# Kernel tuning notes

Hardware: AMD Instinct MI355X
Metric: run time of the kernel (lower is better)

## Reference

```python
import jax, jax.numpy as jnp
import numpy as np

B, S, D, H = 2, 2048, 1024, 16
DH = D // H  # 64


def setup_inputs() -> dict:
    key = jax.random.key(0)
    k1, k2, k3 = jax.random.split(key, 3)
    return {
        "x": jax.random.normal(k1, (B, S, D), dtype=jnp.float32),
        "w_qkv": jax.random.normal(k2, (D, 3 * D), dtype=jnp.float32) * 0.02,
        "b_qkv": jnp.zeros((3 * D,), dtype=jnp.float32),
        "w_out": jax.random.normal(k3, (D, D), dtype=jnp.float32) * 0.02,
        "b_out": jnp.zeros((D,), dtype=jnp.float32),
    }


def reference(x, w_qkv, b_qkv, w_out, b_out):
    # fused qkv projection: [B,S,3D]
    qkv = x @ w_qkv + b_qkv
    q, k, v = qkv[..., :D], qkv[..., D:2 * D], qkv[..., 2 * D:]
    # split heads -> [B,H,S,DH]
    split = lambda t: t.reshape(B, S, H, DH).transpose(0, 2, 1, 3)
    q, k, v = split(q), split(k), split(v)
    scale = 1.0 / jnp.sqrt(jnp.asarray(DH, dtype=x.dtype))
    scores = jnp.einsum("bhqd,bhkd->bhqk", q, k) * scale  # [B,H,S,S]
    attn = jax.nn.softmax(scores, axis=-1)
    out = jnp.einsum("bhqk,bhkd->bhqd", attn, v)  # [B,H,S,DH]
    out = out.transpose(0, 2, 1, 3).reshape(B, S, D)
    return out @ w_out + b_out
```

## Files before the change

kernel.cpp:

```cpp
#include <hip/hip_runtime.h>
#include <cstdint>

#define B_ 2
#define S_ 2048
#define D_ 1024
#define H_ 16
#define DH_ 64

typedef short bf16x8 __attribute__((ext_vector_type(8)));
typedef float f32x4 __attribute__((ext_vector_type(4)));

__device__ inline unsigned short f2bf(float f) {
  unsigned int u = __float_as_uint(f);
  u += 0x7fffu + ((u >> 16) & 1u);
  return (unsigned short)(u >> 16);
}

__device__ inline float bf2f(unsigned short h) {
  return __uint_as_float(((unsigned int)h) << 16);
}

__device__ inline float fexp2(float x) { return __builtin_amdgcn_exp2f(x); }

__device__ inline int swz(int row, int bytecol) {
  return row * 128 + (bytecol ^ ((row & 7) << 4));
}

#define GLL(gp, lp)                                                            \
  __builtin_amdgcn_global_load_lds(                                            \
      (const __attribute__((address_space(1))) unsigned int*)(gp),             \
      (__attribute__((address_space(3))) unsigned int*)(lp), 16, 0, 0)

__global__ __launch_bounds__(256) void k_prep(const float* __restrict__ x,
                                              unsigned short* __restrict__ xb,
                                              const float* __restrict__ w_qkv,
                                              unsigned short* __restrict__ wqT,
                                              const float* __restrict__ w_out,
                                              unsigned short* __restrict__ woT) {
  __shared__ float tile[32][33];
  const int bid = blockIdx.x;
  const int t = threadIdx.x;
  if (bid < 4096) {
    int i = bid * 256 + t;
    float4 v = reinterpret_cast<const float4*>(x)[i];
    ushort4 o;
    o.x = f2bf(v.x); o.y = f2bf(v.y); o.z = f2bf(v.z); o.w = f2bf(v.w);
    reinterpret_cast<ushort4*>(xb)[i] = o;
    return;
  }
  const float* in;
  unsigned short* out;
  int R, C, bx, by;
  if (bid < 7168) {
    int id = bid - 4096;
    bx = id % 96; by = id / 96;
    in = w_qkv; out = wqT; R = 1024; C = 3072;
  } else {
    int id = bid - 7168;
    bx = id & 31; by = id >> 5;
    in = w_out; out = woT; R = 1024; C = 1024;
  }
  int ct = bx * 32, rt = by * 32;
  int tx = t & 31, ty = t >> 5;
#pragma unroll
  for (int i = 0; i < 32; i += 8)
    tile[ty + i][tx] = in[(size_t)(rt + ty + i) * C + ct + tx];
  __syncthreads();
#pragma unroll
  for (int i = 0; i < 32; i += 8)
    out[(size_t)(ct + ty + i) * R + rt + tx] = f2bf(tile[tx][ty + i]);
}

#define READB(p)                                                               \
  _Pragma("unroll") for (int nt = 0; nt < 4; ++nt)                             \
  _Pragma("unroll") for (int ks = 0; ks < 2; ++ks)                             \
      bf[nt][ks] = *(const bf16x8*)((const char*)&Bs[cur][0] +                 \
                   swz((p) * 64 + nt * 16 + ln15, ks * 64 + lg * 16));

#define STAGEPIECE(h)                                                          \
  _Pragma("unroll") for (int j = 0; j < 2; ++j) {                              \
    const int rr = ((h) & 1) * 128 + srow + 64 * j;                            \
    const int gc = scol8 ^ (rr & 7);                                           \
    const unsigned short* gsrc =                                               \
        (((h) < 2) ? (A + (size_t)(row0 + rr) * K)                             \
                   : (BT + (size_t)(col0 + rr) * K)) + k0n + gc * 8;           \
    char* ldst = (char*)(((h) < 2) ? &As[cur ^ 1][0] : &Bs[cur ^ 1][0]) +      \
                 rr * 128 + scol8 * 16;                                        \
    GLL(gsrc, ldst);                                                           \
  }

#define MFMAQ(p)                                                               \
  _Pragma("unroll") for (int mt = 0; mt < 2; ++mt)                             \
  _Pragma("unroll") for (int nt = 0; nt < 4; ++nt) {                           \
    acc[mt][(p) * 4 + nt] = __builtin_amdgcn_mfma_f32_16x16x32_bf16(           \
        af[mt][0], bf[nt][0], acc[mt][(p) * 4 + nt], 0, 0, 0);                 \
    acc[mt][(p) * 4 + nt] = __builtin_amdgcn_mfma_f32_16x16x32_bf16(           \
        af[mt][1], bf[nt][1], acc[mt][(p) * 4 + nt], 0, 0, 0);                 \
  }

template <typename OutT>
__global__ __launch_bounds__(512, 2) void k_gemm8(const unsigned short* __restrict__ A,
                                                  const unsigned short* __restrict__ BT,
                                                  const float* __restrict__ bias,
                                                  OutT* __restrict__ C,
                                                  unsigned short* __restrict__ VTout,
                                                  int M, int N, int K) {
  __shared__ unsigned short As[2][256 * 64];
  __shared__ unsigned short Bs[2][256 * 64];
  const int t = threadIdx.x;
  const int lane = t & 63;
  const int w = t >> 6;
  const int ln15 = lane & 15, lg = lane >> 4;
  const int srow = t >> 3;
  const int scol8 = t & 7;
  const int nwg = gridDim.x * gridDim.y;
  const int flat = blockIdx.y * gridDim.x + blockIdx.x;
  const int cpx = nwg >> 3;
  const int sid = (flat & 7) * cpx + (flat >> 3);
  const int row0 = (sid % gridDim.x) * 256, col0 = (sid / gridDim.x) * 256;

  f32x4 acc[2][16];
#pragma unroll
  for (int i = 0; i < 2; ++i)
#pragma unroll
    for (int j = 0; j < 16; ++j)
      acc[i][j] = (f32x4){0.f, 0.f, 0.f, 0.f};

  const int NTILES = K / 64;
  {
    const int k0n = 0;
    const int cur = 1;
    STAGEPIECE(0); STAGEPIECE(1); STAGEPIECE(2); STAGEPIECE(3);
  }
  asm volatile("s_waitcnt vmcnt(0)" ::: "memory");
  __builtin_amdgcn_s_barrier();

  int cur = 0;
  for (int kt = 0; kt < NTILES; ++kt) {
    const int k0n = (kt + 1) * 64;
    const bool more = (kt + 1) < NTILES;
    bf16x8 af[2][2];
    {
      bf16x8 bf[4][2];
      READB(0);
#pragma unroll
      for (int mt = 0; mt < 2; ++mt)
#pragma unroll
        for (int ks = 0; ks < 2; ++ks)
          af[mt][ks] = *(const bf16x8*)((const char*)&As[cur][0] +
                       swz(w * 32 + mt * 16 + ln15, ks * 64 + lg * 16));
      if (more) { STAGEPIECE(0); }
      __builtin_amdgcn_s_barrier();
      __builtin_amdgcn_s_setprio(1);
      MFMAQ(0);
      __builtin_amdgcn_s_setprio(0);
      __builtin_amdgcn_s_barrier();
    }
    {
      bf16x8 bf[4][2];
      READB(1);
      if (more) {
        STAGEPIECE(1);
        asm volatile("s_waitcnt vmcnt(4)" ::: "memory");
      } else {
        asm volatile("s_waitcnt vmcnt(0)" ::: "memory");
      }
      __builtin_amdgcn_s_barrier();
      __builtin_amdgcn_s_setprio(1);
      MFMAQ(1);
      __builtin_amdgcn_s_setprio(0);
      __builtin_amdgcn_s_barrier();
    }
    {
      bf16x8 bf[4][2];
      READB(2);
      if (more) { STAGEPIECE(2); }
      __builtin_amdgcn_s_barrier();
      __builtin_amdgcn_s_setprio(1);
      MFMAQ(2);
      __builtin_amdgcn_s_setprio(0);
      __builtin_amdgcn_s_barrier();
    }
    {
      bf16x8 bf[4][2];
      READB(3);
      if (more) {
        STAGEPIECE(3);
        asm volatile("s_waitcnt vmcnt(2)" ::: "memory");
      }
      __builtin_amdgcn_s_barrier();
      __builtin_amdgcn_s_setprio(1);
      MFMAQ(3);
      __builtin_amdgcn_s_setprio(0);
      __builtin_amdgcn_s_barrier();
    }
    cur ^= 1;
  }

#pragma unroll
  for (int mt = 0; mt < 2; ++mt) {
#pragma unroll
    for (int nt = 0; nt < 16; ++nt) {
      int col = col0 + nt * 16 + ln15;
      float bv = bias[col];
      if (VTout != nullptr && col >= 2048) {
        int hd = col - 2048;
        int row = row0 + w * 32 + mt * 16 + lg * 4;
        int bb = row >> 11, ss = row & 2047;
        ushort4 o;
        o.x = f2bf(acc[mt][nt][0] + bv);
        o.y = f2bf(acc[mt][nt][1] + bv);
        o.z = f2bf(acc[mt][nt][2] + bv);
        o.w = f2bf(acc[mt][nt][3] + bv);
        *(ushort4*)&VTout[(((size_t)(bb * 16 + (hd >> 6)) * 64) + (hd & 63)) * 2048 + ss] = o;
      } else {
#pragma unroll
        for (int r = 0; r < 4; ++r) {
          int row = row0 + w * 32 + mt * 16 + lg * 4 + r;
          float v = acc[mt][nt][r] + bv;
          if constexpr (sizeof(OutT) == 2)
            C[(size_t)row * N + col] = f2bf(v);
          else
            C[(size_t)row * N + col] = v;
        }
      }
    }
  }
}

template <int BM, int BN, typename OutT>
__global__ __launch_bounds__(256) void k_gemm(const unsigned short* __restrict__ A,
                                              const unsigned short* __restrict__ BT,
                                              const float* __restrict__ bias,
                                              OutT* __restrict__ C,
                                              unsigned short* __restrict__ VTout,
                                              int M, int N, int K) {
  constexpr int MT = BM / 32, NT = BN / 32;
  __shared__ unsigned short As2[BM * 64];
  __shared__ unsigned short Bs2[BN * 64];
  const int t = threadIdx.x;
  const int lane = t & 63;
  const int wave = t >> 6;
  const int wm = wave >> 1, wn = wave & 1;
  const int ln15 = lane & 15, lg = lane >> 4;
  const int nwg = gridDim.x * gridDim.y;
  const int flat = blockIdx.y * gridDim.x + blockIdx.x;
  const int cpx = nwg >> 3;
  const int sid = (flat & 7) * cpx + (flat >> 3);
  const int row0 = (sid % gridDim.x) * BM, col0 = (sid / gridDim.x) * BN;
  f32x4 acc[MT][NT];
#pragma unroll
  for (int i = 0; i < MT; ++i)
#pragma unroll
    for (int j = 0; j < NT; ++j)
      acc[i][j] = (f32x4){0.f, 0.f, 0.f, 0.f};

  for (int k0 = 0; k0 < K; k0 += 64) {
    __syncthreads();
#pragma unroll
    for (int i = 0; i < BM / 32; ++i) {
      int chunk = i * 256 + t;
      int r = chunk >> 3;
      int cb = (chunk & 7) * 16;
      GLL((const char*)(A + (size_t)(row0 + r) * K + k0) + cb, (char*)As2 + chunk * 16);
    }
#pragma unroll
    for (int i = 0; i < BN / 32; ++i) {
      int chunk = i * 256 + t;
      int r = chunk >> 3;
      int cb = (chunk & 7) * 16;
      GLL((const char*)(BT + (size_t)(col0 + r) * K + k0) + cb, (char*)Bs2 + chunk * 16);
    }
    __syncthreads();
#pragma unroll
    for (int ks = 0; ks < 2; ++ks) {
      bf16x8 af[MT], bf[NT];
#pragma unroll
      for (int mt = 0; mt < MT; ++mt)
        af[mt] = *(const bf16x8*)&As2[(wm * (BM / 2) + mt * 16 + ln15) * 64 + ks * 32 + lg * 8];
#pragma unroll
      for (int nt = 0; nt < NT; ++nt)
        bf[nt] = *(const bf16x8*)&Bs2[(wn * (BN / 2) + nt * 16 + ln15) * 64 + ks * 32 + lg * 8];
#pragma unroll
      for (int mt = 0; mt < MT; ++mt)
#pragma unroll
        for (int nt = 0; nt < NT; ++nt)
          acc[mt][nt] = __builtin_amdgcn_mfma_f32_16x16x32_bf16(af[mt], bf[nt], acc[mt][nt], 0, 0, 0);
    }
  }
#pragma unroll
  for (int mt = 0; mt < MT; ++mt) {
#pragma unroll
    for (int nt = 0; nt < NT; ++nt) {
      int col = col0 + wn * (BN / 2) + nt * 16 + ln15;
      float bv = bias[col];
#pragma unroll
      for (int r = 0; r < 4; ++r) {
        int row = row0 + wm * (BM / 2) + mt * 16 + lg * 4 + r;
        float v = acc[mt][nt][r] + bv;
        if constexpr (sizeof(OutT) == 2)
          C[(size_t)row * N + col] = f2bf(v);
        else
          C[(size_t)row * N + col] = v;
      }
    }
  }
}

__global__ __launch_bounds__(512) void k_attn(const unsigned short* __restrict__ qkv,
                                              const unsigned short* __restrict__ VT,
                                              unsigned short* __restrict__ O) {
  __shared__ unsigned short Ks[2][64 * 64];
  __shared__ unsigned short Vs[2][64 * 64];
  __shared__ unsigned short Ps[8][16 * 64];

  const int bid = blockIdx.x;
  const int xcd = bid & 7, idx = bid >> 3;
  const int bh = xcd + (idx >> 4) * 8;
  const int qblk = idx & 15;
  const int b = bh >> 4, h = bh & 15;
  const int t = threadIdx.x, wave = t >> 6, lane = t & 63;
  const int ln15 = lane & 15, lg = lane >> 4;
  const unsigned short* Qb = qkv + (size_t)b * S_ * 3072 + h * 64;
  const unsigned short* Kb = Qb + 1024;
  const unsigned short* Vb = VT + (size_t)bh * 64 * 2048;
  const int q0 = qblk * 128 + wave * 16;

  const float qsc = 0.125f * 1.4426950408889634f;
  bf16x8 qf[2];
#pragma unroll
  for (int ks = 0; ks < 2; ++ks) {
    bf16x8 raw = *(const bf16x8*)&Qb[(size_t)(q0 + ln15) * 3072 + ks * 32 + lg * 8];
#pragma unroll
    for (int j = 0; j < 8; ++j)
      qf[ks][j] = (short)f2bf(bf2f((unsigned short)raw[j]) * qsc);
  }

  const int srow = t >> 3;
  const int scol = (t & 7) ^ (srow & 7);
  const unsigned short* kPtr0 = Kb + (size_t)srow * 3072 + scol * 8;
  const unsigned short* vPtr0 = Vb + (size_t)srow * 2048 + scol * 8;
  char* ldsK0 = (char*)&Ks[0][0] + t * 16;
  char* ldsV0 = (char*)&Vs[0][0] + t * 16;

  auto stage = [&](int bi, int kv) {
    GLL(kPtr0 + (size_t)kv * 3072, ldsK0 + bi * 8192);
    GLL(vPtr0 + kv, ldsV0 + bi * 8192);
  };

  f32x4 acc[4];
#pragma unroll
  for (int dt = 0; dt < 4; ++dt)
    acc[dt] = (f32x4){0.f, 0.f, 0.f, 0.f};
  float m0 = -1e30f, l0 = 0.f;
  unsigned short* Pw = Ps[wave];

  stage(0, 0);
  __syncthreads();
  int buf = 0;

  for (int kv = 0; kv < S_; kv += 64) {
    if (kv + 64 < S_) stage(buf ^ 1, kv + 64);

    f32x4 st[4];
#pragma unroll
    for (int kg = 0; kg < 4; ++kg)
      st[kg] = (f32x4){0.f, 0.f, 0.f, 0.f};
    __builtin_amdgcn_s_setprio(1);
#pragma unroll
    for (int kg = 0; kg < 4; ++kg) {
      int krow = kg * 16 + ln15;
      bf16x8 kf0 = *(const bf16x8*)((const char*)&Ks[buf][0] + swz(krow, lg * 16));
      bf16x8 kf1 = *(const bf16x8*)((const char*)&Ks[buf][0] + swz(krow, 64 + lg * 16));
      st[kg] = __builtin_amdgcn_mfma_f32_16x16x32_bf16(kf0, qf[0], st[kg], 0, 0, 0);
      st[kg] = __builtin_amdgcn_mfma_f32_16x16x32_bf16(kf1, qf[1], st[kg], 0, 0, 0);
    }
    __builtin_amdgcn_s_setprio(0);

    float tm = -1e30f;
#pragma unroll
    for (int kg = 0; kg < 4; ++kg)
      tm = fmaxf(tm, fmaxf(fmaxf(st[kg][0], st[kg][1]),
                           fmaxf(st[kg][2], st[kg][3])));
    tm = fmaxf(tm, __shfl_xor(tm, 16));
    tm = fmaxf(tm, __shfl_xor(tm, 32));

    if (__any(tm > m0 + 11.0f)) {
      float n0 = fmaxf(m0, tm);
      float r0 = fexp2(m0 - n0);
      m0 = n0; l0 *= r0;
#pragma unroll
      for (int dt = 0; dt < 4; ++dt)
#pragma unroll
        for (int r = 0; r < 4; ++r)
          acc[dt][r] *= r0;
    }

    asm volatile("" ::: "memory");
    float ts = 0.f;
#pragma unroll
    for (int kg = 0; kg < 4; ++kg) {
      float p0 = fexp2(st[kg][0] - m0);
      float p1 = fexp2(st[kg][1] - m0);
      float p2 = fexp2(st[kg][2] - m0);
      float p3 = fexp2(st[kg][3] - m0);
      ts += (p0 + p1) + (p2 + p3);
      unsigned int w0, w1;
      asm("v_cvt_pk_bf16_f32 %0, %1, %2" : "=v"(w0) : "v"(p0), "v"(p1));
      asm("v_cvt_pk_bf16_f32 %0, %1, %2" : "=v"(w1) : "v"(p2), "v"(p3));
      *(uint2*)((char*)Pw + swz(ln15, kg * 32 + lg * 8)) = make_uint2(w0, w1);
    }
    ts += __shfl_xor(ts, 16);
    ts += __shfl_xor(ts, 32);
    l0 += ts;
    asm volatile("" ::: "memory");

    __builtin_amdgcn_s_setprio(1);
#pragma unroll
    for (int kc = 0; kc < 2; ++kc) {
      bf16x8 pf = *(const bf16x8*)((const char*)Pw + swz(ln15, kc * 64 + lg * 16));
#pragma unroll
      for (int dt = 0; dt < 4; ++dt) {
        bf16x8 vf = *(const bf16x8*)((const char*)&Vs[buf][0] + swz(dt * 16 + ln15, kc * 64 + lg * 16));
        acc[dt] = __builtin_amdgcn_mfma_f32_16x16x32_bf16(vf, pf, acc[dt], 0, 0, 0);
      }
    }
    __builtin_amdgcn_s_setprio(0);
    __syncthreads();
    buf ^= 1;
  }

  float inv = 1.f / l0;
  size_t qglob = q0 + ln15;
  size_t base = ((size_t)b * S_ + qglob) * D_ + h * 64 + lg * 4;
#pragma unroll
  for (int dt = 0; dt < 4; ++dt) {
    ushort4 o;
    o.x = f2bf(acc[dt][0] * inv);
    o.y = f2bf(acc[dt][1] * inv);
    o.z = f2bf(acc[dt][2] * inv);
    o.w = f2bf(acc[dt][3] * inv);
    *(ushort4*)&O[base + (size_t)dt * 16] = o;
  }
}

extern "C" void kernel_launch(void* const* d_in, const int* in_sizes, int n_in,
                              void* d_out, int out_size, void* d_ws, size_t ws_size,
                              hipStream_t stream) {
  const float* x     = (const float*)d_in[0];
  const float* w_qkv = (const float*)d_in[1];
  const float* b_qkv = (const float*)d_in[2];
  const float* w_out = (const float*)d_in[3];
  const float* b_out = (const float*)d_in[4];
  float* out = (float*)d_out;

  char* ws = (char*)d_ws;
  const size_t MiB = (size_t)1 << 20;
  unsigned short* xb   = (unsigned short*)(ws + 0 * MiB);
  unsigned short* wqT  = (unsigned short*)(ws + 8 * MiB);
  unsigned short* woT  = (unsigned short*)(ws + 14 * MiB);
  unsigned short* qkvb = (unsigned short*)(ws + 16 * MiB);
  unsigned short* VTb  = (unsigned short*)(ws + 40 * MiB);
  unsigned short* Ab   = (unsigned short*)(ws + 48 * MiB);

  k_prep<<<8192, 256, 0, stream>>>(x, xb, w_qkv, wqT, w_out, woT);
  k_gemm8<unsigned short><<<dim3(16, 12), 512, 0, stream>>>(xb, wqT, b_qkv, qkvb, VTb, 4096, 3072, 1024);
  k_attn<<<512, 512, 0, stream>>>(qkvb, VTb, Ab);
  k_gemm<128, 64, float><<<dim3(32, 16), 256, 0, stream>>>(Ab, woT, b_out, out, nullptr, 4096, 1024, 1024);
}
```

Measured before the change: 200.9 us.

## Retile QKV GEMM to 256x192, halve attention blocks, defer row-sum reduction

The QKV GEMM tile changes from 256x256 to 256x192, which raises the grid from 192 to 256 workgroups so it fills the CUs more evenly. The A and B staging is restructured to match, with new wait counts. The attention kernel now uses 256-thread blocks covering 64 queries each, doubling the block count, and each thread stages two chunks per K/V tile. The softmax row-sum shuffle reduction moves out of the KV loop to the end. The risks are lower reuse per tile in the GEMM and hand-tuned vmcnt values that could be wrong.

```diff
diff --git a/kernel.cpp b/kernel.cpp
--- a/kernel.cpp
+++ b/kernel.cpp
@@ -71,42 +71,42 @@
     out[(size_t)(ct + ty + i) * R + rt + tx] = f2bf(tile[tx][ty + i]);
 }
 
-#define READB(p)                                                               \
-  _Pragma("unroll") for (int nt = 0; nt < 4; ++nt)                             \
+#define STAGE_A(h)                                                             \
+  {                                                                            \
+    const int rr = (h) * 64 + srow;                                            \
+    const int gc = scol8 ^ (rr & 7);                                           \
+    GLL(A + (size_t)(row0 + rr) * K + k0n + gc * 8,                            \
+        (char*)&As[cur ^ 1][0] + rr * 128 + scol8 * 16);                       \
+  }
+#define STAGE_B(h)                                                             \
+  {                                                                            \
+    const int rr = (h) * 64 + srow;                                            \
+    const int gc = scol8 ^ (rr & 7);                                           \
+    GLL(BT + (size_t)(col0 + rr) * K + k0n + gc * 8,                           \
+        (char*)&Bs[cur ^ 1][0] + rr * 128 + scol8 * 16);                       \
+  }
+#define READB3(p)                                                              \
+  _Pragma("unroll") for (int nt = 0; nt < 3; ++nt)                             \
   _Pragma("unroll") for (int ks = 0; ks < 2; ++ks)                             \
       bf[nt][ks] = *(const bf16x8*)((const char*)&Bs[cur][0] +                 \
-                   swz((p) * 64 + nt * 16 + ln15, ks * 64 + lg * 16));
-
-#define STAGEPIECE(h)                                                          \
-  _Pragma("unroll") for (int j = 0; j < 2; ++j) {                              \
-    const int rr = ((h) & 1) * 128 + srow + 64 * j;                            \
-    const int gc = scol8 ^ (rr & 7);                                           \
-    const unsigned short* gsrc =                                               \
-        (((h) < 2) ? (A + (size_t)(row0 + rr) * K)                             \
-                   : (BT + (size_t)(col0 + rr) * K)) + k0n + gc * 8;           \
-    char* ldst = (char*)(((h) < 2) ? &As[cur ^ 1][0] : &Bs[cur ^ 1][0]) +      \
-                 rr * 128 + scol8 * 16;                                        \
-    GLL(gsrc, ldst);                                                           \
-  }
-
-#define MFMAQ(p)                                                               \
+                   swz((p) * 48 + nt * 16 + ln15, ks * 64 + lg * 16));
+#define MFMAQ3(p)                                                              \
   _Pragma("unroll") for (int mt = 0; mt < 2; ++mt)                             \
-  _Pragma("unroll") for (int nt = 0; nt < 4; ++nt) {                           \
-    acc[mt][(p) * 4 + nt] = __builtin_amdgcn_mfma_f32_16x16x32_bf16(           \
-        af[mt][0], bf[nt][0], acc[mt][(p) * 4 + nt], 0, 0, 0);                 \
-    acc[mt][(p) * 4 + nt] = __builtin_amdgcn_mfma_f32_16x16x32_bf16(           \
-        af[mt][1], bf[nt][1], acc[mt][(p) * 4 + nt], 0, 0, 0);                 \
-  }
-
-template <typename OutT>
+  _Pragma("unroll") for (int nt = 0; nt < 3; ++nt) {                           \
+    acc[mt][(p) * 3 + nt] = __builtin_amdgcn_mfma_f32_16x16x32_bf16(           \
+        af[mt][0], bf[nt][0], acc[mt][(p) * 3 + nt], 0, 0, 0);                 \
+    acc[mt][(p) * 3 + nt] = __builtin_amdgcn_mfma_f32_16x16x32_bf16(           \
+        af[mt][1], bf[nt][1], acc[mt][(p) * 3 + nt], 0, 0, 0);                 \
+  }
+
 __global__ __launch_bounds__(512, 2) void k_gemm8(const unsigned short* __restrict__ A,
                                                   const unsigned short* __restrict__ BT,
                                                   const float* __restrict__ bias,
-                                                  OutT* __restrict__ C,
+                                                  unsigned short* __restrict__ C,
                                                   unsigned short* __restrict__ VTout,
                                                   int M, int N, int K) {
   __shared__ unsigned short As[2][256 * 64];
-  __shared__ unsigned short Bs[2][256 * 64];
+  __shared__ unsigned short Bs[2][192 * 64];
   const int t = threadIdx.x;
   const int lane = t & 63;
   const int w = t >> 6;
@@ -117,20 +117,21 @@
   const int flat = blockIdx.y * gridDim.x + blockIdx.x;
   const int cpx = nwg >> 3;
   const int sid = (flat & 7) * cpx + (flat >> 3);
-  const int row0 = (sid % gridDim.x) * 256, col0 = (sid / gridDim.x) * 256;
-
-  f32x4 acc[2][16];
+  const int row0 = (sid % gridDim.x) * 256, col0 = (sid / gridDim.x) * 192;
+
+  f32x4 acc[2][12];
 #pragma unroll
   for (int i = 0; i < 2; ++i)
 #pragma unroll
-    for (int j = 0; j < 16; ++j)
+    for (int j = 0; j < 12; ++j)
       acc[i][j] = (f32x4){0.f, 0.f, 0.f, 0.f};
 
   const int NTILES = K / 64;
   {
     const int k0n = 0;
     const int cur = 1;
-    STAGEPIECE(0); STAGEPIECE(1); STAGEPIECE(2); STAGEPIECE(3);
+    STAGE_A(0); STAGE_A(1); STAGE_A(2); STAGE_A(3);
+    STAGE_B(0); STAGE_B(1); STAGE_B(2);
   }
   asm volatile("s_waitcnt vmcnt(0)" ::: "memory");
   __builtin_amdgcn_s_barrier();
@@ -141,56 +142,59 @@
     const bool more = (kt + 1) < NTILES;
     bf16x8 af[2][2];
     {
-      bf16x8 bf[4][2];
-      READB(0);
+      bf16x8 bf[3][2];
+      READB3(0);
 #pragma unroll
       for (int mt = 0; mt < 2; ++mt)
 #pragma unroll
         for (int ks = 0; ks < 2; ++ks)
           af[mt][ks] = *(const bf16x8*)((const char*)&As[cur][0] +
                        swz(w * 32 + mt * 16 + ln15, ks * 64 + lg * 16));
-      if (more) { STAGEPIECE(0); }
+      if (more) { STAGE_A(0); STAGE_A(1); }
       __builtin_amdgcn_s_barrier();
       __builtin_amdgcn_s_setprio(1);
-      MFMAQ(0);
+      MFMAQ3(0);
       __builtin_amdgcn_s_setprio(0);
       __builtin_amdgcn_s_barrier();
     }
     {
-      bf16x8 bf[4][2];
-      READB(1);
+      bf16x8 bf[3][2];
+      READB3(1);
       if (more) {
-        STAGEPIECE(1);
-        asm volatile("s_waitcnt vmcnt(4)" ::: "memory");
+        STAGE_A(2); STAGE_A(3);
+        asm volatile("s_waitcnt vmcnt(5)" ::: "memory");
       } else {
         asm volatile("s_waitcnt vmcnt(0)" ::: "memory");
       }
       __builtin_amdgcn_s_barrier();
       __builtin_amdgcn_s_setprio(1);
-      MFMAQ(1);
+      MFMAQ3(1);
       __builtin_amdgcn_s_setprio(0);
       __builtin_amdgcn_s_barrier();
     }
     {
-      bf16x8 bf[4][2];
-      READB(2);
-      if (more) { STAGEPIECE(2); }
+      bf16x8 bf[3][2];
+      READB3(2);
+      if (more) {
+        STAGE_B(0); STAGE_B(1);
+        asm volatile("s_waitcnt vmcnt(6)" ::: "memory");
+      }
       __builtin_amdgcn_s_barrier();
       __builtin_amdgcn_s_setprio(1);
-      MFMAQ(2);
+      MFMAQ3(2);
       __builtin_amdgcn_s_setprio(0);
       __builtin_amdgcn_s_barrier();
     }
     {
-      bf16x8 bf[4][2];
-      READB(3);
+      bf16x8 bf[3][2];
+      READB3(3);
       if (more) {
-        STAGEPIECE(3);
+        STAGE_B(2);
         asm volatile("s_waitcnt vmcnt(2)" ::: "memory");
       }
       __builtin_amdgcn_s_barrier();
       __builtin_amdgcn_s_setprio(1);
-      MFMAQ(3);
+      MFMAQ3(3);
       __builtin_amdgcn_s_setprio(0);
       __builtin_amdgcn_s_barrier();
     }
@@ -200,10 +204,10 @@
 #pragma unroll
   for (int mt = 0; mt < 2; ++mt) {
 #pragma unroll
-    for (int nt = 0; nt < 16; ++nt) {
+    for (int nt = 0; nt < 12; ++nt) {
       int col = col0 + nt * 16 + ln15;
       float bv = bias[col];
-      if (VTout != nullptr && col >= 2048) {
+      if (col >= 2048) {
         int hd = col - 2048;
         int row = row0 + w * 32 + mt * 16 + lg * 4;
         int bb = row >> 11, ss = row & 2047;
@@ -217,11 +221,7 @@
 #pragma unroll
         for (int r = 0; r < 4; ++r) {
           int row = row0 + w * 32 + mt * 16 + lg * 4 + r;
-          float v = acc[mt][nt][r] + bv;
-          if constexpr (sizeof(OutT) == 2)
-            C[(size_t)row * N + col] = f2bf(v);
-          else
-            C[(size_t)row * N + col] = v;
+          C[(size_t)row * N + col] = f2bf(acc[mt][nt][r] + bv);
         }
       }
     }
@@ -233,7 +233,6 @@
                                               const unsigned short* __restrict__ BT,
                                               const float* __restrict__ bias,
                                               OutT* __restrict__ C,
-                                              unsigned short* __restrict__ VTout,
                                               int M, int N, int K) {
   constexpr int MT = BM / 32, NT = BN / 32;
   __shared__ unsigned short As2[BM * 64];
@@ -307,24 +306,24 @@
   }
 }
 
-__global__ __launch_bounds__(512) void k_attn(const unsigned short* __restrict__ qkv,
+__global__ __launch_bounds__(256) void k_attn(const unsigned short* __restrict__ qkv,
                                               const unsigned short* __restrict__ VT,
                                               unsigned short* __restrict__ O) {
   __shared__ unsigned short Ks[2][64 * 64];
   __shared__ unsigned short Vs[2][64 * 64];
-  __shared__ unsigned short Ps[8][16 * 64];
+  __shared__ unsigned short Ps[4][16 * 64];
 
   const int bid = blockIdx.x;
   const int xcd = bid & 7, idx = bid >> 3;
-  const int bh = xcd + (idx >> 4) * 8;
-  const int qblk = idx & 15;
+  const int bh = xcd + (idx >> 5) * 8;
+  const int qblk = idx & 31;
   const int b = bh >> 4, h = bh & 15;
   const int t = threadIdx.x, wave = t >> 6, lane = t & 63;
   const int ln15 = lane & 15, lg = lane >> 4;
   const unsigned short* Qb = qkv + (size_t)b * S_ * 3072 + h * 64;
   const unsigned short* Kb = Qb + 1024;
   const unsigned short* Vb = VT + (size_t)bh * 64 * 2048;
-  const int q0 = qblk * 128 + wave * 16;
+  const int q0 = qblk * 64 + wave * 16;
 
   const float qsc = 0.125f * 1.4426950408889634f;
   bf16x8 qf[2];
@@ -345,7 +344,9 @@
 
   auto stage = [&](int bi, int kv) {
     GLL(kPtr0 + (size_t)kv * 3072, ldsK0 + bi * 8192);
+    GLL(kPtr0 + (size_t)(kv + 32) * 3072, ldsK0 + bi * 8192 + 4096);
     GLL(vPtr0 + kv, ldsV0 + bi * 8192);
+    GLL(vPtr0 + kv + (size_t)32 * 2048, ldsV0 + bi * 8192 + 4096);
   };
 
   f32x4 acc[4];
@@ -397,22 +398,18 @@
     }
 
     asm volatile("" ::: "memory");
-    float ts = 0.f;
 #pragma unroll
     for (int kg = 0; kg < 4; ++kg) {
       float p0 = fexp2(st[kg][0] - m0);
       float p1 = fexp2(st[kg][1] - m0);
       float p2 = fexp2(st[kg][2] - m0);
       float p3 = fexp2(st[kg][3] - m0);
-      ts += (p0 + p1) + (p2 + p3);
+      l0 += (p0 + p1) + (p2 + p3);
       unsigned int w0, w1;
       asm("v_cvt_pk_bf16_f32 %0, %1, %2" : "=v"(w0) : "v"(p0), "v"(p1));
       asm("v_cvt_pk_bf16_f32 %0, %1, %2" : "=v"(w1) : "v"(p2), "v"(p3));
       *(uint2*)((char*)Pw + swz(ln15, kg * 32 + lg * 8)) = make_uint2(w0, w1);
     }
-    ts += __shfl_xor(ts, 16);
-    ts += __shfl_xor(ts, 32);
-    l0 += ts;
     asm volatile("" ::: "memory");
 
     __builtin_amdgcn_s_setprio(1);
@@ -430,6 +427,8 @@
     buf ^= 1;
   }
 
+  l0 += __shfl_xor(l0, 16);
+  l0 += __shfl_xor(l0, 32);
   float inv = 1.f / l0;
   size_t qglob = q0 + ln15;
   size_t base = ((size_t)b * S_ + qglob) * D_ + h * 64 + lg * 4;
@@ -464,7 +463,7 @@
   unsigned short* Ab   = (unsigned short*)(ws + 48 * MiB);
 
   k_prep<<<8192, 256, 0, stream>>>(x, xb, w_qkv, wqT, w_out, woT);
-  k_gemm8<unsigned short><<<dim3(16, 12), 512, 0, stream>>>(xb, wqT, b_qkv, qkvb, VTb, 4096, 3072, 1024);
-  k_attn<<<512, 512, 0, stream>>>(qkvb, VTb, Ab);
-  k_gemm<128, 64, float><<<dim3(32, 16), 256, 0, stream>>>(Ab, woT, b_out, out, nullptr, 4096, 1024, 1024);
-}
+  k_gemm8<<<dim3(16, 16), 512, 0, stream>>>(xb, wqT, b_qkv, qkvb, VTb, 4096, 3072, 1024);
+  k_attn<<<1024, 256, 0, stream>>>(qkvb, VTb, Ab);
+  k_gemm<128, 64, float><<<dim3(32, 16), 256, 0, stream>>>(Ab, woT, b_out, out, 4096, 1024, 1024);
+}
```

Measured after the change: 205.9 us. +2.5%, slower.
